# Optimization experiments

Measured on AMD Instinct MI355X. Metric: run time of the kernel, lower is better.

Reference implementation:

```python
import jax, jax.numpy as jnp
import numpy as np


def _time_encoding(t, hidden_dim):
    # Sinusoidal continuous-time encoding: t [B,T] -> [B,T,H]
    half = hidden_dim // 2
    freqs = jnp.exp(-jnp.arange(half, dtype=t.dtype) * (np.log(10000.0) / half))
    ang = t[..., None] * freqs  # [B,T,half]
    return jnp.concatenate([jnp.sin(ang), jnp.cos(ang)], axis=-1)


def _gru(x_tbh, w_ih, w_hh, b_ih, b_hh):
    # PyTorch-convention GRU over time-major input [T,B,H]
    B = x_tbh.shape[1]
    H = w_hh.shape[1]
    h0 = jnp.zeros((B, H), x_tbh.dtype)

    def step(h, x):
        gi = x @ w_ih.T + b_ih
        gh = h @ w_hh.T + b_hh
        i_r, i_z, i_n = jnp.split(gi, 3, axis=-1)
        h_r, h_z, h_n = jnp.split(gh, 3, axis=-1)
        r = jax.nn.sigmoid(i_r + h_r)
        z = jax.nn.sigmoid(i_z + h_z)
        n = jnp.tanh(i_n + r * h_n)
        h_new = (1.0 - z) * n + z * h
        return h_new, h_new

    _, ys = jax.lax.scan(step, h0, x_tbh)
    return ys  # [T,B,H]


def setup_inputs():
    key = jax.random.key(0)
    ks = jax.random.split(key, 8)
    B, T, D, H = 32, 256, 64, 128
    x = jax.random.normal(ks[0], (B, T, D), jnp.float32)
    missing_mask = (jax.random.uniform(ks[1], (B, T, D)) < 0.5).astype(jnp.float32)
    visit_time = jnp.cumsum(jax.random.uniform(ks[2], (B, T), jnp.float32) * 2.0, axis=1)
    time_delta = jnp.zeros((B, T), jnp.float32)
    lengths = jax.random.randint(ks[3], (B,), T // 2, T + 1).astype(jnp.int32)
    lengths = lengths.at[0].set(T)  # pad_packed returns max(lengths) steps; pin to T
    sensor_embed = jax.random.normal(ks[4], (D, H), jnp.float32) * 0.02
    k = 1.0 / np.sqrt(H)
    gru_w_ih = jax.random.uniform(ks[5], (3 * H, H), jnp.float32, -k, k)
    gru_w_hh = jax.random.uniform(ks[6], (3 * H, H), jnp.float32, -k, k)
    gru_b_ih = jax.random.uniform(ks[7], (3 * H,), jnp.float32, -k, k)
    gru_b_hh = jnp.zeros((3 * H,), jnp.float32)
    return dict(x=x, missing_mask=missing_mask, visit_time=visit_time,
                time_delta=time_delta, lengths=lengths, sensor_embed=sensor_embed,
                gru_w_ih=gru_w_ih, gru_w_hh=gru_w_hh, gru_b_ih=gru_b_ih, gru_b_hh=gru_b_hh)


def reference(x, missing_mask, visit_time, time_delta, lengths, sensor_embed,
              gru_w_ih, gru_w_hh, gru_b_ih, gru_b_hh):
    B, T, D = x.shape
    H = sensor_embed.shape[1]
    observed = 1.0 - missing_mask                                   # [B,T,D]
    # sensor tokens: per-(t,sensor) embedding scaled by value, zeroed if missing
    sensor_tokens = x[..., None] * sensor_embed[None, None] * observed[..., None]  # [B,T,D,H]
    presence = observed.mean(axis=1)                                # [B,D]
    sim = jax.nn.relu(sensor_embed @ sensor_embed.T)                # [D,D]
    adj = presence[:, :, None] * presence[:, None, :] * sim[None]   # [B,D,D]
    adj = adj + jnp.eye(D, dtype=x.dtype)[None]
    adj = adj / jnp.maximum(adj.sum(axis=-1, keepdims=True), 1e-6)
    graph_tokens = jnp.einsum('bij,btjh->btih', adj, sensor_tokens) # [B,T,D,H]
    visit_repr = graph_tokens.mean(axis=2) + _time_encoding(visit_time, H)  # [B,T,H]
    # dropout is identity in eval mode
    ys = _gru(jnp.swapaxes(visit_repr, 0, 1), gru_w_ih, gru_w_hh, gru_b_ih, gru_b_hh)
    out = jnp.swapaxes(ys, 0, 1)                                    # [B,T,H]
    # pad_packed_sequence semantics: zeros beyond each sequence length
    mask = (jnp.arange(T)[None, :] < lengths[:, None])[..., None]
    return out * mask
```

## Files before the change

kernel.cpp:

```cpp
#include <hip/hip_runtime.h>
#include <hip/hip_bf16.h>

#define B_ 32
#define T_ 256
#define D_ 64
#define H_ 128
#define G_ 384

typedef _Float16 half8 __attribute__((ext_vector_type(8)));
typedef _Float16 half4v __attribute__((ext_vector_type(4)));
typedef float float4v __attribute__((ext_vector_type(4)));

__device__ __forceinline__ float fsigmoid(float x){ return 1.0f/(1.0f+__expf(-x)); }
__device__ __forceinline__ float ftanh_(float x){ return 1.0f - 2.0f/(1.0f+__expf(2.0f*x)); }

#define BAR() do{ asm volatile("s_waitcnt lgkmcnt(0)" ::: "memory"); \
                  __builtin_amdgcn_s_barrier(); \
                  asm volatile("" ::: "memory"); } while(0)

__global__ void __launch_bounds__(256) adj_k(const float* mm, const float* E,
                                             float* wcol){
  int b = blockIdx.x;
  int tid = threadIdx.x;
  int d = tid & 63, q = tid >> 6;
  __shared__ float spp[4][64];
  __shared__ float sp[64];
  __shared__ float sE[64*129];
  __shared__ float ssim[64*65];
  __shared__ float srs[64];
  float p = 0.0f;
  for (int t = q*64; t < q*64+64; t++) p += 1.0f - mm[(b*T_ + t)*D_ + d];
  spp[q][d] = p;
  for (int i = tid; i < D_*H_; i += 256){ int r = i >> 7, c = i & 127; sE[r*129+c] = E[i]; }
  __syncthreads();
  if (tid < 64) sp[tid] = (spp[0][tid]+spp[1][tid]+spp[2][tid]+spp[3][tid]) * (1.0f/T_);
  __syncthreads();
  float rowE[128];
  #pragma unroll
  for (int k = 0; k < 128; k++) rowE[k] = sE[d*129+k];
  for (int i = q*16; i < q*16+16; i++){
    float s = 0.0f;
    #pragma unroll
    for (int k = 0; k < 128; k++) s += rowE[k]*sE[i*129+k];
    ssim[d*65+i] = fmaxf(s, 0.0f);
  }
  __syncthreads();
  if (tid < 64){
    float rs = 0.0f;
    for (int j = 0; j < 64; j++) rs += sp[j]*ssim[tid*65+j];
    srs[tid] = fmaxf(sp[tid]*rs + 1.0f, 1e-6f);
  }
  __syncthreads();
  if (tid < 64){
    float s = 0.0f;
    for (int i = 0; i < 64; i++) s += sp[i]*ssim[tid*65+i]/srs[i];
    wcol[b*64 + tid] = sp[tid]*s + 1.0f/srs[tid];
  }
}

#define AVP 72
#define VRP 136
#define SEP 132
__global__ void __launch_bounds__(512,1) gi_k(const float* x, const float* mm,
                                              const float* vt, const float* E,
                                              const float* wih, const float* bih,
                                              const float* bhh, const float* wcol,
                                              _Float16* gi3){
  int bid = blockIdx.x;
  int b = bid >> 3, t0 = (bid & 7)*32;
  int tid = threadIdx.x;
  int w = tid >> 6, l = tid & 63;
  int lq = l >> 4, lm = l & 15;

  __shared__ __align__(16) _Float16 av[32*AVP];
  __shared__ __align__(16) _Float16 vrA[32*VRP];
  __shared__ __align__(16) _Float16 sEl[64*SEP];
  __shared__ float sVt[32];

  {
    int i = tid*4, t = i >> 6, d4 = i & 63;
    long src = (long)(b*T_ + t0 + t)*D_ + d4;
    float4 xv = *(const float4*)&x[src];
    float4 mv = *(const float4*)&mm[src];
    float4 wv = *(const float4*)&wcol[b*D_ + d4];
    half4v h;
    h[0]=(_Float16)(xv.x*(1.0f-mv.x)*wv.x*(1.0f/64));
    h[1]=(_Float16)(xv.y*(1.0f-mv.y)*wv.y*(1.0f/64));
    h[2]=(_Float16)(xv.z*(1.0f-mv.z)*wv.z*(1.0f/64));
    h[3]=(_Float16)(xv.w*(1.0f-mv.w)*wv.w*(1.0f/64));
    *(half4v*)&av[t*AVP + d4] = h;
  }
  {
    int r = tid >> 3, c0 = (tid & 7)*16;
    #pragma unroll
    for (int g = 0; g < 4; g++){
      float4 v = *(const float4*)&E[r*H_ + c0 + g*4];
      half4v h;
      h[0]=(_Float16)v.x; h[1]=(_Float16)v.y; h[2]=(_Float16)v.z; h[3]=(_Float16)v.w;
      *(half4v*)&sEl[r*SEP + c0 + g*4] = h;
    }
  }
  if (tid < 32) sVt[tid] = vt[b*T_ + t0 + tid];
  __syncthreads();

  half8 bE[2];
  #pragma unroll
  for (int kc = 0; kc < 2; kc++){
    half8 f;
    #pragma unroll
    for (int jj = 0; jj < 8; jj++)
      f[jj] = sEl[(kc*32 + lq*8 + jj)*SEP + 16*w + lm];
    bE[kc] = f;
  }

  float4v accA[2] = {{0,0,0,0},{0,0,0,0}};
  #pragma unroll
  for (int kc = 0; kc < 2; kc++){
    #pragma unroll
    for (int mt = 0; mt < 2; mt++){
      half8 a = *(const half8*)&av[(mt*16+lm)*AVP + kc*32 + lq*8];
      accA[mt] = __builtin_amdgcn_mfma_f32_16x16x32_f16(a, bE[kc], accA[mt], 0,0,0);
    }
  }
  {
    int h = 16*w + lm;
    float fr = __expf(-(float)(h & 63) * 0.14391157f);
    #pragma unroll
    for (int mt = 0; mt < 2; mt++){
      #pragma unroll
      for (int r = 0; r < 4; r++){
        int tl = mt*16 + lq*4 + r;
        float ang = sVt[tl] * fr;
        float e = (h < 64) ? __sinf(ang) : __cosf(ang);
        vrA[tl*VRP + h] = (_Float16)(accA[mt][r] + e);
      }
    }
  }
  __syncthreads();

  half8 bW[3][4]; float biW[3];
  #pragma unroll
  for (int q = 0; q < 3; q++){
    int g = 16*(3*w + q) + lm;
    biW[q] = bih[g] + (g < 2*H_ ? bhh[g] : 0.0f);
    #pragma unroll
    for (int kc = 0; kc < 4; kc++){
      const float* src = &wih[(long)g*H_ + kc*32 + lq*8];
      float4 x0 = *(const float4*)src;
      float4 x1 = *(const float4*)(src+4);
      half8 f;
      f[0]=(_Float16)x0.x; f[1]=(_Float16)x0.y; f[2]=(_Float16)x0.z; f[3]=(_Float16)x0.w;
      f[4]=(_Float16)x1.x; f[5]=(_Float16)x1.y; f[6]=(_Float16)x1.z; f[7]=(_Float16)x1.w;
      bW[q][kc] = f;
    }
  }
  float4v cB[2][3];
  #pragma unroll
  for (int mt = 0; mt < 2; mt++)
    #pragma unroll
    for (int q = 0; q < 3; q++) cB[mt][q] = (float4v){0,0,0,0};
  #pragma unroll
  for (int kc = 0; kc < 4; kc++){
    #pragma unroll
    for (int mt = 0; mt < 2; mt++){
      half8 a = *(const half8*)&vrA[(mt*16+lm)*VRP + kc*32 + lq*8];
      #pragma unroll
      for (int q = 0; q < 3; q++)
        cB[mt][q] = __builtin_amdgcn_mfma_f32_16x16x32_f16(a, bW[q][kc], cB[mt][q], 0,0,0);
    }
  }
  #pragma unroll
  for (int mt = 0; mt < 2; mt++){
    #pragma unroll
    for (int q = 0; q < 3; q++){
      int g = 16*(3*w + q) + lm;
      int tb = t0 + mt*16 + lq*4;
      half4v hv;
      hv[0]=(_Float16)(cB[mt][q][0] + biW[q]); hv[1]=(_Float16)(cB[mt][q][1] + biW[q]);
      hv[2]=(_Float16)(cB[mt][q][2] + biW[q]); hv[3]=(_Float16)(cB[mt][q][3] + biW[q]);
      *(half4v*)&gi3[((long)(b*G_ + g))*T_ + tb] = hv;
    }
  }
}

__global__ void __launch_bounds__(256,1) gru_k(const _Float16* gi3, const float* whh,
                                               const float* bhh, const int* lengths,
                                               float* out){
  int b = blockIdx.x;
  int tid = threadIdx.x;
  int w = tid >> 6, l = tid & 63;
  int lq = l >> 4, lm = l & 15;
  int len = lengths[b];
  bool gate = (l < 32);
  int j = 32*w + l;

  __shared__ __align__(16) _Float16 hb[2][H_];

  half8 bfrag[6][4];
  #pragma unroll
  for (int i = 0; i < 6; i++){
    int row = 32*w + (i>>1)*H_ + (i&1)*16 + lm;
    #pragma unroll
    for (int kc = 0; kc < 4; kc++){
      const float* src = &whh[(long)row*H_ + kc*32 + lq*8];
      float4 x0 = *(const float4*)src;
      float4 x1 = *(const float4*)(src+4);
      half8 f;
      f[0]=(_Float16)x0.x; f[1]=(_Float16)x0.y; f[2]=(_Float16)x0.z; f[3]=(_Float16)x0.w;
      f[4]=(_Float16)x1.x; f[5]=(_Float16)x1.y; f[6]=(_Float16)x1.z; f[7]=(_Float16)x1.w;
      bfrag[i][kc] = f;
    }
  }
  float bn_ = 0.0f;
  const _Float16* pr = nullptr; const _Float16* pz; const _Float16* pn;
  if (gate){
    bn_ = bhh[2*H_ + j];
    pr = gi3 + ((long)b*G_ + j)*T_;
    pz = pr + (long)H_*T_;
    pn = pr + (long)2*H_*T_;
  }
  if (tid < H_){ hb[0][tid] = (_Float16)0.0f; hb[1][tid] = (_Float16)0.0f; }

  float gr[2][8], gz[2][8], gn[2][8];
  if (gate){
    half8 a = *(const half8*)(pr);
    half8 bv = *(const half8*)(pz);
    half8 cv = *(const half8*)(pn);
    #pragma unroll
    for (int i = 0; i < 8; i++){ gr[0][i]=(float)a[i]; gz[0][i]=(float)bv[i]; gn[0][i]=(float)cv[i]; }
  }
  __syncthreads();

  float hval = 0.0f;
  float ho[8];
  int cb = 0;
  for (int c = 0; c < 32; c++){
    if (gate && c+1 < 32){
      int nb2 = (c+1)*8;
      half8 a = *(const half8*)(pr+nb2);
      half8 bv = *(const half8*)(pz+nb2);
      half8 cv = *(const half8*)(pn+nb2);
      int nc = cb^1;
      #pragma unroll
      for (int i = 0; i < 8; i++){ gr[nc][i]=(float)a[i]; gz[nc][i]=(float)bv[i]; gn[nc][i]=(float)cv[i]; }
    }
    #pragma unroll
    for (int i = 0; i < 8; i++){
      int rp = i & 1;
      half8 a0v = *(const half8*)&hb[rp][0*32 + lq*8];
      half8 a1v = *(const half8*)&hb[rp][1*32 + lq*8];
      half8 a2v = *(const half8*)&hb[rp][2*32 + lq*8];
      half8 a3v = *(const half8*)&hb[rp][3*32 + lq*8];
      float4v cc[6];
      #pragma unroll
      for (int q = 0; q < 6; q++) cc[q] = (float4v){0,0,0,0};
      #pragma unroll
      for (int q = 0; q < 6; q++) cc[q] = __builtin_amdgcn_mfma_f32_16x16x32_f16(a0v, bfrag[q][0], cc[q], 0,0,0);
      #pragma unroll
      for (int q = 0; q < 6; q++) cc[q] = __builtin_amdgcn_mfma_f32_16x16x32_f16(a1v, bfrag[q][1], cc[q], 0,0,0);
      #pragma unroll
      for (int q = 0; q < 6; q++) cc[q] = __builtin_amdgcn_mfma_f32_16x16x32_f16(a2v, bfrag[q][2], cc[q], 0,0,0);
      #pragma unroll
      for (int q = 0; q < 6; q++) cc[q] = __builtin_amdgcn_mfma_f32_16x16x32_f16(a3v, bfrag[q][3], cc[q], 0,0,0);
      float ghr = (l & 16) ? cc[1][0] : cc[0][0];
      float ghz = (l & 16) ? cc[3][0] : cc[2][0];
      float ghn = (l & 16) ? cc[5][0] : cc[4][0];
      if (gate){
        float r = fsigmoid(gr[cb][i] + ghr);
        float z = fsigmoid(gz[cb][i] + ghz);
        float n = ftanh_(gn[cb][i] + r*(ghn + bn_));
        hval = (1.0f - z)*n + z*hval;
        hb[rp^1][j] = (_Float16)hval;
        ho[i] = (c*8 + i < len) ? hval : 0.0f;
      }
      BAR();
    }
    if (gate){
      long ob = ((long)b*T_ + c*8)*H_ + j;
      #pragma unroll
      for (int i = 0; i < 8; i++) out[ob + (long)i*H_] = ho[i];
    }
    cb ^= 1;
  }
}

extern "C" void kernel_launch(void* const* d_in, const int* in_sizes, int n_in,
                              void* d_out, int out_size, void* d_ws, size_t ws_size,
                              hipStream_t stream) {
  char* base = (char*)d_ws;
  size_t off = 0;
  auto alloc = [&](size_t bytes)->void*{
    void* p = base + off; off = (off + bytes + 255) & ~(size_t)255; return p;
  };
  float*     wcol = (float*)alloc((size_t)B_*D_*4);
  _Float16*  gi3  = (_Float16*)alloc((size_t)B_*G_*T_*2);
  if (off > ws_size) return;

  const float* x   = (const float*)d_in[0];
  const float* mm  = (const float*)d_in[1];
  const float* vt  = (const float*)d_in[2];
  const int*   len = (const int*)d_in[4];
  const float* E   = (const float*)d_in[5];
  const float* wih = (const float*)d_in[6];
  const float* whh = (const float*)d_in[7];
  const float* bih = (const float*)d_in[8];
  const float* bhh = (const float*)d_in[9];

  adj_k<<<dim3(B_),dim3(256),0,stream>>>(mm, E, wcol);
  gi_k<<<dim3(256),dim3(512),0,stream>>>(x, mm, vt, E, wih, bih, bhh, wcol, gi3);
  gru_k<<<dim3(B_),dim3(256),0,stream>>>(gi3, whh, bhh, len, (float*)d_out);
}
```

Baseline: 253.5 us.

## Replace MFMA recurrent matvec with per-thread fdot2 over register-resident weights

The GRU recurrence kernel drops the 16x16x32 MFMA tiles, which wasted most of their output on a batch-one matvec. Instead each pair of threads owns one hidden unit and holds half of its three weight rows as packed fp16 in registers. Each thread computes its partial dot products with v_dot2 and the pair combines them with one lane shuffle. This is meant to shorten the per-step critical path, at the cost of 96 packed weight registers per thread and broadcast LDS reads of the hidden state.

```diff
diff --git a/kernel.cpp b/kernel.cpp
--- a/kernel.cpp
+++ b/kernel.cpp
@@ -9,6 +9,7 @@
 
 typedef _Float16 half8 __attribute__((ext_vector_type(8)));
 typedef _Float16 half4v __attribute__((ext_vector_type(4)));
+typedef _Float16 half2v __attribute__((ext_vector_type(2)));
 typedef float float4v __attribute__((ext_vector_type(4)));
 
 __device__ __forceinline__ float fsigmoid(float x){ return 1.0f/(1.0f+__expf(-x)); }
@@ -188,41 +189,36 @@
                                                float* out){
   int b = blockIdx.x;
   int tid = threadIdx.x;
-  int w = tid >> 6, l = tid & 63;
-  int lq = l >> 4, lm = l & 15;
+  int j  = tid >> 1;
+  int kh = tid & 1;
   int len = lengths[b];
-  bool gate = (l < 32);
-  int j = 32*w + l;
+  bool even = (kh == 0);
 
   __shared__ __align__(16) _Float16 hb[2][H_];
 
-  half8 bfrag[6][4];
-  #pragma unroll
-  for (int i = 0; i < 6; i++){
-    int row = 32*w + (i>>1)*H_ + (i&1)*16 + lm;
-    #pragma unroll
-    for (int kc = 0; kc < 4; kc++){
-      const float* src = &whh[(long)row*H_ + kc*32 + lq*8];
-      float4 x0 = *(const float4*)src;
-      float4 x1 = *(const float4*)(src+4);
-      half8 f;
-      f[0]=(_Float16)x0.x; f[1]=(_Float16)x0.y; f[2]=(_Float16)x0.z; f[3]=(_Float16)x0.w;
-      f[4]=(_Float16)x1.x; f[5]=(_Float16)x1.y; f[6]=(_Float16)x1.z; f[7]=(_Float16)x1.w;
-      bfrag[i][kc] = f;
-    }
-  }
-  float bn_ = 0.0f;
-  const _Float16* pr = nullptr; const _Float16* pz; const _Float16* pn;
-  if (gate){
-    bn_ = bhh[2*H_ + j];
-    pr = gi3 + ((long)b*G_ + j)*T_;
-    pz = pr + (long)H_*T_;
-    pn = pr + (long)2*H_*T_;
-  }
+  half2v Wr[3][32];
+  #pragma unroll
+  for (int s = 0; s < 3; s++){
+    const float* src = &whh[(long)(s*H_ + j)*H_ + kh*64];
+    #pragma unroll
+    for (int q4 = 0; q4 < 16; q4++){
+      float4 v = *(const float4*)(src + q4*4);
+      half2v a, c;
+      a[0]=(_Float16)v.x; a[1]=(_Float16)v.y;
+      c[0]=(_Float16)v.z; c[1]=(_Float16)v.w;
+      Wr[s][2*q4]   = a;
+      Wr[s][2*q4+1] = c;
+    }
+  }
+  float bn_ = bhh[2*H_ + j];
+  const _Float16* pr = gi3 + ((long)b*G_ + j)*T_;
+  const _Float16* pz = pr + (long)H_*T_;
+  const _Float16* pn = pr + (long)2*H_*T_;
+
   if (tid < H_){ hb[0][tid] = (_Float16)0.0f; hb[1][tid] = (_Float16)0.0f; }
 
   float gr[2][8], gz[2][8], gn[2][8];
-  if (gate){
+  if (even){
     half8 a = *(const half8*)(pr);
     half8 bv = *(const half8*)(pz);
     half8 cv = *(const half8*)(pn);
@@ -235,7 +231,7 @@
   float ho[8];
   int cb = 0;
   for (int c = 0; c < 32; c++){
-    if (gate && c+1 < 32){
+    if (even && c+1 < 32){
       int nb2 = (c+1)*8;
       half8 a = *(const half8*)(pr+nb2);
       half8 bv = *(const half8*)(pz+nb2);
@@ -247,35 +243,38 @@
     #pragma unroll
     for (int i = 0; i < 8; i++){
       int rp = i & 1;
-      half8 a0v = *(const half8*)&hb[rp][0*32 + lq*8];
-      half8 a1v = *(const half8*)&hb[rp][1*32 + lq*8];
-      half8 a2v = *(const half8*)&hb[rp][2*32 + lq*8];
-      half8 a3v = *(const half8*)&hb[rp][3*32 + lq*8];
-      float4v cc[6];
-      #pragma unroll
-      for (int q = 0; q < 6; q++) cc[q] = (float4v){0,0,0,0};
-      #pragma unroll
-      for (int q = 0; q < 6; q++) cc[q] = __builtin_amdgcn_mfma_f32_16x16x32_f16(a0v, bfrag[q][0], cc[q], 0,0,0);
-      #pragma unroll
-      for (int q = 0; q < 6; q++) cc[q] = __builtin_amdgcn_mfma_f32_16x16x32_f16(a1v, bfrag[q][1], cc[q], 0,0,0);
-      #pragma unroll
-      for (int q = 0; q < 6; q++) cc[q] = __builtin_amdgcn_mfma_f32_16x16x32_f16(a2v, bfrag[q][2], cc[q], 0,0,0);
-      #pragma unroll
-      for (int q = 0; q < 6; q++) cc[q] = __builtin_amdgcn_mfma_f32_16x16x32_f16(a3v, bfrag[q][3], cc[q], 0,0,0);
-      float ghr = (l & 16) ? cc[1][0] : cc[0][0];
-      float ghz = (l & 16) ? cc[3][0] : cc[2][0];
-      float ghn = (l & 16) ? cc[5][0] : cc[4][0];
-      if (gate){
-        float r = fsigmoid(gr[cb][i] + ghr);
-        float z = fsigmoid(gz[cb][i] + ghz);
-        float n = ftanh_(gn[cb][i] + r*(ghn + bn_));
+      float a0[2] = {0.0f, 0.0f};
+      float a1[2] = {0.0f, 0.0f};
+      float a2[2] = {0.0f, 0.0f};
+      #pragma unroll
+      for (int q8 = 0; q8 < 8; q8++){
+        half8 hv = *(const half8*)&hb[rp][kh*64 + q8*8];
+        #pragma unroll
+        for (int m = 0; m < 4; m++){
+          half2v hh; hh[0] = hv[2*m]; hh[1] = hv[2*m+1];
+          int q = q8*4 + m, u = q & 1;
+          a0[u] = __builtin_amdgcn_fdot2(hh, Wr[0][q], a0[u], false);
+          a1[u] = __builtin_amdgcn_fdot2(hh, Wr[1][q], a1[u], false);
+          a2[u] = __builtin_amdgcn_fdot2(hh, Wr[2][q], a2[u], false);
+        }
+      }
+      float R = a0[0] + a0[1];
+      float Z = a1[0] + a1[1];
+      float N = a2[0] + a2[1];
+      R += __shfl_xor(R, 1, 64);
+      Z += __shfl_xor(Z, 1, 64);
+      N += __shfl_xor(N, 1, 64);
+      if (even){
+        float r = fsigmoid(gr[cb][i] + R);
+        float z = fsigmoid(gz[cb][i] + Z);
+        float n = ftanh_(gn[cb][i] + r*(N + bn_));
         hval = (1.0f - z)*n + z*hval;
         hb[rp^1][j] = (_Float16)hval;
         ho[i] = (c*8 + i < len) ? hval : 0.0f;
       }
       BAR();
     }
-    if (gate){
+    if (even){
       long ob = ((long)b*T_ + c*8)*H_ + j;
       #pragma unroll
       for (int i = 0; i < 8; i++) out[ob + (long)i*H_] = ho[i];
```

After: 271.9 us. 7.2% more time.
